# Kernel tuning notes

Hardware: AMD Instinct MI355X
Metric: run time of the kernel (lower is better)

The kernel has to match this reference:

```python
import jax, jax.numpy as jnp
import numpy as np

# Bahdanau additive attention (eval mode: dropout is identity):
#   fac1 = W @ k        [B, d, S]
#   fac2 = U @ q        [B, d, S]
#   s    = v^T tanh(fac1 + fac2)   [B, 1, S]
#   attn = softmax(s, axis=-1)

B, D, S = 32, 1024, 2048


def setup_inputs() -> dict:
    key = jax.random.key(0)
    kq, kk, kv, kW, kU = jax.random.split(key, 5)
    scale = 1.0 / np.sqrt(D)
    return {
        "q": jax.random.normal(kq, (B, D, S), dtype=jnp.float32),
        "k": jax.random.normal(kk, (B, D, S), dtype=jnp.float32),
        "v": jax.random.normal(kv, (B, D, 1), dtype=jnp.float32),
        "W": jax.random.normal(kW, (D, D), dtype=jnp.float32) * scale,
        "U": jax.random.normal(kU, (D, D), dtype=jnp.float32) * scale,
    }


def reference(q, k, v, W, U):
    # projections: [d,e] x [b,e,s] -> [b,d,s]
    fac1 = jnp.einsum("de,bes->bds", W, k)
    fac2 = jnp.einsum("de,bes->bds", U, q)
    e = jnp.tanh(fac1 + fac2)            # [B, D, S]
    s = jnp.einsum("bdo,bds->bos", v, e)  # [B, 1, S]
    attn = jax.nn.softmax(s, axis=-1)     # softmax over sequence
    return attn
```

## Files before the change

### kernel.cpp

```cpp
#include <hip/hip_runtime.h>

#define D_ 1024
#define S_ 2048
#define B_ 32
#define BM 256
#define BN 256
#define BK 64
#define NKT 32

typedef __attribute__((ext_vector_type(8))) _Float16 f16x8;
typedef __attribute__((ext_vector_type(16))) float f32x16;

__device__ __forceinline__ void async_ld16(const void* g, void* l) {
  __builtin_amdgcn_global_load_lds(
      (const __attribute__((address_space(1))) void*)g,
      (__attribute__((address_space(3))) void*)l, 16, 0, 0);
}

__global__ void prep_kernel(const float* __restrict__ W, const float* __restrict__ U,
                            _Float16* __restrict__ wf, _Float16* __restrict__ uf) {
  int t = blockIdx.x * blockDim.x + threadIdx.x;
  const float* src = blockIdx.y ? U : W;
  _Float16* dst = blockIdx.y ? uf : wf;

  int tile = t >> 11;
  int g    = t & 2047;
  int top  = g >> 6;
  int ks = top >> 3, wr = (top >> 2) & 1, fm = top & 3;
  int lane = g & 63, l31 = lane & 31, lhi = lane >> 5;
  int row   = wr * 128 + fm * 32 + l31;
  int chunk = ks * 2 + lhi;
  int d = (tile >> 4) * 256 + row;
  int e = (tile & 15) * 64 + chunk * 8;

  const float* p = src + (size_t)d * D_ + e;
  f16x8 hv;
#pragma unroll
  for (int j = 0; j < 8; ++j) hv[j] = (_Float16)p[j];
  *(f16x8*)(dst + (size_t)t * 8) = hv;
}

__global__ void __launch_bounds__(512, 2)
gemm_kernel(const float* __restrict__ kten, const float* __restrict__ qten,
            const float* __restrict__ v,
            const _Float16* __restrict__ wf, const _Float16* __restrict__ uf,
            float* __restrict__ partials) {
  __shared__ __align__(16) _Float16 Af[2][BM * BK];
  __shared__ __align__(16) _Float16 Bf[2][BN * BK];
  __shared__ float vbuf[BM];
  __shared__ float red[2][BN];

  const int tid  = threadIdx.x;
  const int lane = tid & 63;
  const int wid  = tid >> 6;
  const int wr   = wid >> 2;
  const int wc   = wid & 3;

  int bid  = blockIdx.x;
  int g    = ((bid >> 5) << 3) | (bid & 7);
  int dblk = (bid >> 3) & 3;
  int st   = g & 7;
  int b    = g >> 3;
  int s0   = st * BN;

  if (tid < BM) vbuf[tid] = v[(size_t)b * D_ + dblk * BM + tid];

  f32x16 acc[4][2];
#pragma unroll
  for (int i = 0; i < 4; ++i)
#pragma unroll
    for (int j = 0; j < 2; ++j)
#pragma unroll
      for (int r = 0; r < 16; ++r) acc[i][j][r] = 0.0f;

  const int nB = tid & 255;
  const int kq = tid >> 8;

#define PH_FENCE asm volatile("" ::: "memory")
#define PH_BAR __builtin_amdgcn_s_barrier()

#define GLLA(ktn, buf, part) do {                                              \
    const int half_ = (ktn) >> 4, ktt_ = (ktn) & 15;                           \
    const _Float16* at_ = (half_ ? uf : wf) + (size_t)(dblk * 16 + ktt_) * 16384; \
    async_ld16(at_ + (size_t)(tid + (part) * 1024) * 8,                        \
               &Af[buf][(size_t)(tid + (part) * 1024) * 8]);                   \
    async_ld16(at_ + (size_t)(tid + (part) * 1024 + 512) * 8,                  \
               &Af[buf][(size_t)(tid + (part) * 1024 + 512) * 8]);             \
  } while (0)

#define LOADB(ktn, xv, h) do {                                                 \
    const int half_ = (ktn) >> 4, ktt_ = (ktn) & 15;                           \
    const float* col_ = (half_ ? qten : kten) + (size_t)b * (D_ * S_)          \
                        + (size_t)(ktt_ * 64) * S_ + s0 + nB                   \
                        + (size_t)(kq * 32) * S_;                              \
    _Pragma("unroll")                                                          \
    for (int j = 16 * (h); j < 16 * (h) + 16; ++j) xv[j] = col_[(size_t)j * S_]; \
  } while (0)

#define CVTWRITE(xv, buf) do {                                                 \
    _Pragma("unroll")                                                          \
    for (int cl = 0; cl < 4; ++cl) {                                           \
      f16x8 hv_;                                                               \
      _Pragma("unroll")                                                        \
      for (int w = 0; w < 8; ++w) hv_[w] = (_Float16)xv[cl * 8 + w];           \
      int c_ = kq * 4 + cl, cks_ = c_ >> 1, clh_ = c_ & 1;                     \
      int gnl_ = ((cks_ * 8 + (nB >> 6) * 2 + ((nB >> 5) & 1)) << 6)           \
                 | (clh_ << 5) | (nB & 31);                                    \
      *(f16x8*)&Bf[buf][(size_t)gnl_ * 8] = hv_;                               \
    }                                                                          \
  } while (0)

#define COMPUTE_PHASE(cur_, ks_) do {                                          \
    f16x8 af_[4], bf_[2];                                                      \
    _Pragma("unroll")                                                          \
    for (int fm = 0; fm < 4; ++fm)                                             \
      af_[fm] = *(const f16x8*)&Af[cur_][(size_t)(((ks_) * 8 + wr * 4 + fm) * 64 + lane) * 8]; \
    _Pragma("unroll")                                                          \
    for (int fn = 0; fn < 2; ++fn)                                             \
      bf_[fn] = *(const f16x8*)&Bf[cur_][(size_t)(((ks_) * 8 + wc * 2 + fn) * 64 + lane) * 8]; \
    __builtin_amdgcn_s_setprio(1);                                             \
    _Pragma("unroll")                                                          \
    for (int fm = 0; fm < 4; ++fm)                                             \
      _Pragma("unroll")                                                        \
      for (int fn = 0; fn < 2; ++fn)                                           \
        acc[fm][fn] = __builtin_amdgcn_mfma_f32_32x32x16_f16(af_[fm], bf_[fn], acc[fm][fn], 0, 0, 0); \
    __builtin_amdgcn_s_setprio(0);                                             \
  } while (0)

#define STEP(kt_, cur_, xvC_, xvN_) do {                                       \
    const int nxt_ = (cur_) ^ 1;                                               \
    PH_FENCE; GLLA((kt_) + 1, nxt_, 0); COMPUTE_PHASE(cur_, 0); PH_BAR;        \
    PH_FENCE; GLLA((kt_) + 1, nxt_, 1); COMPUTE_PHASE(cur_, 1); PH_BAR;        \
    PH_FENCE; LOADB((kt_) + 2, xvN_, 0); COMPUTE_PHASE(cur_, 2); PH_BAR;       \
    PH_FENCE; LOADB((kt_) + 2, xvN_, 1); CVTWRITE(xvC_, nxt_);                 \
              COMPUTE_PHASE(cur_, 3);                                          \
    asm volatile("s_waitcnt vmcnt(32) lgkmcnt(0)" ::: "memory");               \
    PH_BAR;                                                                    \
    __builtin_amdgcn_sched_barrier(0);                                         \
  } while (0)

  float xvA[32], xvB[32];
  LOADB(0, xvA, 0); LOADB(0, xvA, 1);
  GLLA(0, 0, 0);    GLLA(0, 0, 1);
  LOADB(1, xvB, 0); LOADB(1, xvB, 1);
  CVTWRITE(xvA, 0);
  __syncthreads();

  for (int it = 0; it < 15; ++it) {
    STEP(2 * it,     0, xvB, xvA);
    STEP(2 * it + 1, 1, xvA, xvB);
  }

  PH_FENCE; GLLA(31, 1, 0); COMPUTE_PHASE(0, 0); PH_BAR;
  PH_FENCE; GLLA(31, 1, 1); COMPUTE_PHASE(0, 1); PH_BAR;
  PH_FENCE; COMPUTE_PHASE(0, 2); PH_BAR;
  PH_FENCE; CVTWRITE(xvB, 1); COMPUTE_PHASE(0, 3);
  __syncthreads();
  COMPUTE_PHASE(1, 0); COMPUTE_PHASE(1, 1); COMPUTE_PHASE(1, 2); COMPUTE_PHASE(1, 3);

#undef STEP
#undef COMPUTE_PHASE
#undef CVTWRITE
#undef LOADB
#undef GLLA
#undef PH_BAR
#undef PH_FENCE

  float psum[2] = {0.f, 0.f};
#pragma unroll
  for (int fm = 0; fm < 4; ++fm)
#pragma unroll
    for (int fn = 0; fn < 2; ++fn)
#pragma unroll
      for (int r = 0; r < 16; ++r) {
        int row = wr * 128 + fm * 32 + (r & 3) + 8 * (r >> 2) + 4 * (lane >> 5);
        float x  = acc[fm][fn][r];
        float th = 1.0f - 2.0f / (__expf(2.0f * x) + 1.0f);
        psum[fn] += vbuf[row] * th;
      }
#pragma unroll
  for (int fn = 0; fn < 2; ++fn) psum[fn] += __shfl_xor(psum[fn], 32);
  if (lane < 32) {
    red[wr][wc * 64 + lane]      = psum[0];
    red[wr][wc * 64 + 32 + lane] = psum[1];
  }
  __syncthreads();
  if (tid < BN) {
    float val = red[0][tid] + red[1][tid];
    partials[(size_t)(dblk * B_ + b) * S_ + s0 + tid] = val;
  }
}

__global__ void softmax_kernel(const float* __restrict__ partials, float* __restrict__ out) {
  __shared__ float logit[S_];
  __shared__ float wred[2][4];
  int b = blockIdx.x, tid = threadIdx.x;
  int lane = tid & 63, wid = tid >> 6;
  float lmax = -1e30f;
  for (int i = tid; i < S_; i += 256) {
    float acc = 0.f;
#pragma unroll
    for (int d = 0; d < 4; ++d) acc += partials[(size_t)(d * B_ + b) * S_ + i];
    logit[i] = acc;
    lmax = fmaxf(lmax, acc);
  }
#pragma unroll
  for (int o = 32; o; o >>= 1) lmax = fmaxf(lmax, __shfl_xor(lmax, o));
  if (lane == 0) wred[0][wid] = lmax;
  __syncthreads();
  float m = fmaxf(fmaxf(wred[0][0], wred[0][1]), fmaxf(wred[0][2], wred[0][3]));
  float lsum = 0.f;
  for (int i = tid; i < S_; i += 256) {
    float ex = __expf(logit[i] - m);
    logit[i] = ex;
    lsum += ex;
  }
#pragma unroll
  for (int o = 32; o; o >>= 1) lsum += __shfl_xor(lsum, o);
  if (lane == 0) wred[1][wid] = lsum;
  __syncthreads();
  float tot = wred[1][0] + wred[1][1] + wred[1][2] + wred[1][3];
  float inv = 1.0f / tot;
  for (int i = tid; i < S_; i += 256) out[(size_t)b * S_ + i] = logit[i] * inv;
}

extern "C" void kernel_launch(void* const* d_in, const int* in_sizes, int n_in,
                              void* d_out, int out_size, void* d_ws, size_t ws_size,
                              hipStream_t stream) {
  const float* q = (const float*)d_in[0];
  const float* k = (const float*)d_in[1];
  const float* v = (const float*)d_in[2];
  const float* W = (const float*)d_in[3];
  const float* U = (const float*)d_in[4];

  _Float16* wf = (_Float16*)d_ws;
  _Float16* uf = wf + (size_t)D_ * D_;
  float* partials = (float*)(uf + (size_t)D_ * D_);

  prep_kernel<<<dim3(512, 2), 256, 0, stream>>>(W, U, wf, uf);
  gemm_kernel<<<dim3(1024), 512, 0, stream>>>(k, q, v, wf, uf, partials);
  softmax_kernel<<<dim3(B_), 256, 0, stream>>>(partials, (float*)d_out);
}
```

Before: 401.3 us.

## Pre-convert k/q to fp16 MFMA layout and stream B tiles via async LDS loads

Adds a separate pass that converts the k and q activations to fp16 and writes them in the MFMA fragment layout in workspace. The GEMM then loads both A and B tiles with global-to-LDS async loads and a simpler double-buffered pipeline, dropping the per-thread fp32 register loads and in-kernel conversion. The cost is an extra full read of 512 MB of fp32 plus a 256 MB fp16 write and read back. The old path is kept as a fallback when the workspace is too small.

```diff
diff --git a/kernel.cpp b/kernel.cpp
--- a/kernel.cpp
+++ b/kernel.cpp
@@ -40,10 +40,32 @@
   *(f16x8*)(dst + (size_t)t * 8) = hv;
 }
 
+__global__ void kqprep_kernel(const float* __restrict__ kten, const float* __restrict__ qten,
+                              _Float16* __restrict__ bfmt) {
+  size_t t = (size_t)blockIdx.x * 256 + threadIdx.x;
+  int g    = (int)(t & 2047);
+  int tile = (int)(t >> 11);
+  int st   = tile & 7;
+  int ktt  = (tile >> 3) & 15;
+  int half = (tile >> 7) & 1;
+  int b    = tile >> 8;
+  int l31 = g & 31, clh = (g >> 5) & 1, w2 = (g >> 6) & 7, cks = g >> 9;
+  int n = w2 * 32 + l31;
+  int c = cks * 2 + clh;
+  int e = ktt * 64 + c * 8;
+  int s = st * 256 + n;
+
+  const float* src = (half ? qten : kten) + (size_t)b * (D_ * S_) + (size_t)e * S_ + s;
+  f16x8 hv;
+#pragma unroll
+  for (int j = 0; j < 8; ++j) hv[j] = (_Float16)src[(size_t)j * S_];
+  *(f16x8*)(bfmt + t * 8) = hv;
+}
+
 __global__ void __launch_bounds__(512, 2)
-gemm_kernel(const float* __restrict__ kten, const float* __restrict__ qten,
-            const float* __restrict__ v,
+gemm_kernel(const float* __restrict__ v,
             const _Float16* __restrict__ wf, const _Float16* __restrict__ uf,
+            const _Float16* __restrict__ bfmt,
             float* __restrict__ partials) {
   __shared__ __align__(16) _Float16 Af[2][BM * BK];
   __shared__ __align__(16) _Float16 Bf[2][BN * BK];
@@ -73,13 +95,9 @@
 #pragma unroll
       for (int r = 0; r < 16; ++r) acc[i][j][r] = 0.0f;
 
-  const int nB = tid & 255;
-  const int kq = tid >> 8;
-
 #define PH_FENCE asm volatile("" ::: "memory")
-#define PH_BAR __builtin_amdgcn_s_barrier()
-
-#define GLLA(ktn, buf, part) do {                                              \
+
+#define GLLA2(ktn, buf, part) do {                                             \
     const int half_ = (ktn) >> 4, ktt_ = (ktn) & 15;                           \
     const _Float16* at_ = (half_ ? uf : wf) + (size_t)(dblk * 16 + ktt_) * 16384; \
     async_ld16(at_ + (size_t)(tid + (part) * 1024) * 8,                        \
@@ -88,7 +106,142 @@
                &Af[buf][(size_t)(tid + (part) * 1024 + 512) * 8]);             \
   } while (0)
 
-#define LOADB(ktn, xv, h) do {                                                 \
+#define GLLB2(ktn, buf, part) do {                                             \
+    const int half_ = (ktn) >> 4, ktt_ = (ktn) & 15;                           \
+    const _Float16* bt_ = bfmt + ((size_t)(((b * 2 + half_) * 16 + ktt_) * 8 + st)) * 16384; \
+    async_ld16(bt_ + (size_t)(tid + (part) * 1024) * 8,                        \
+               &Bf[buf][(size_t)(tid + (part) * 1024) * 8]);                   \
+    async_ld16(bt_ + (size_t)(tid + (part) * 1024 + 512) * 8,                  \
+               &Bf[buf][(size_t)(tid + (part) * 1024 + 512) * 8]);             \
+  } while (0)
+
+#define COMPUTE_PHASE(cur_, ks_) do {                                          \
+    f16x8 af_[4], bf_[2];                                                      \
+    _Pragma("unroll")                                                          \
+    for (int fm = 0; fm < 4; ++fm)                                             \
+      af_[fm] = *(const f16x8*)&Af[cur_][(size_t)(((ks_) * 8 + wr * 4 + fm) * 64 + lane) * 8]; \
+    _Pragma("unroll")                                                          \
+    for (int fn = 0; fn < 2; ++fn)                                             \
+      bf_[fn] = *(const f16x8*)&Bf[cur_][(size_t)(((ks_) * 8 + wc * 2 + fn) * 64 + lane) * 8]; \
+    __builtin_amdgcn_s_setprio(1);                                             \
+    _Pragma("unroll")                                                          \
+    for (int fm = 0; fm < 4; ++fm)                                             \
+      _Pragma("unroll")                                                        \
+      for (int fn = 0; fn < 2; ++fn)                                           \
+        acc[fm][fn] = __builtin_amdgcn_mfma_f32_32x32x16_f16(af_[fm], bf_[fn], acc[fm][fn], 0, 0, 0); \
+    __builtin_amdgcn_s_setprio(0);                                             \
+  } while (0)
+
+#define WAIT_BAR(n) do {                                                       \
+    asm volatile("s_waitcnt vmcnt(" #n ")" ::: "memory");                      \
+    __builtin_amdgcn_s_barrier();                                              \
+    __builtin_amdgcn_sched_barrier(0);                                         \
+  } while (0)
+
+  PH_FENCE;
+  GLLA2(0, 0, 0); GLLB2(0, 0, 0);
+  GLLA2(0, 0, 1); GLLB2(0, 0, 1);
+  WAIT_BAR(4);
+
+  for (int kt = 0; kt < NKT - 1; ++kt) {
+    const int cur = kt & 1, nxt = cur ^ 1;
+    PH_FENCE;
+    GLLA2(kt + 1, nxt, 0); GLLB2(kt + 1, nxt, 0);
+    COMPUTE_PHASE(cur, 0);
+    COMPUTE_PHASE(cur, 1);
+    WAIT_BAR(4);
+    PH_FENCE;
+    GLLA2(kt + 1, nxt, 1); GLLB2(kt + 1, nxt, 1);
+    COMPUTE_PHASE(cur, 2);
+    COMPUTE_PHASE(cur, 3);
+    WAIT_BAR(4);
+  }
+  COMPUTE_PHASE(1, 0);
+  COMPUTE_PHASE(1, 1);
+  WAIT_BAR(0);
+  COMPUTE_PHASE(1, 2);
+  COMPUTE_PHASE(1, 3);
+
+#undef WAIT_BAR
+#undef COMPUTE_PHASE
+#undef GLLB2
+#undef GLLA2
+#undef PH_FENCE
+
+  float psum[2] = {0.f, 0.f};
+#pragma unroll
+  for (int fm = 0; fm < 4; ++fm)
+#pragma unroll
+    for (int fn = 0; fn < 2; ++fn)
+#pragma unroll
+      for (int r = 0; r < 16; ++r) {
+        int row = wr * 128 + fm * 32 + (r & 3) + 8 * (r >> 2) + 4 * (lane >> 5);
+        float x  = acc[fm][fn][r];
+        float th = 1.0f - 2.0f / (__expf(2.0f * x) + 1.0f);
+        psum[fn] += vbuf[row] * th;
+      }
+#pragma unroll
+  for (int fn = 0; fn < 2; ++fn) psum[fn] += __shfl_xor(psum[fn], 32);
+  if (lane < 32) {
+    red[wr][wc * 64 + lane]      = psum[0];
+    red[wr][wc * 64 + 32 + lane] = psum[1];
+  }
+  __syncthreads();
+  if (tid < BN) {
+    float val = red[0][tid] + red[1][tid];
+    partials[(size_t)(dblk * B_ + b) * S_ + s0 + tid] = val;
+  }
+}
+
+__global__ void __launch_bounds__(512, 2)
+gemm_fb_kernel(const float* __restrict__ kten, const float* __restrict__ qten,
+               const float* __restrict__ v,
+               const _Float16* __restrict__ wf, const _Float16* __restrict__ uf,
+               float* __restrict__ partials) {
+  __shared__ __align__(16) _Float16 Af[2][BM * BK];
+  __shared__ __align__(16) _Float16 Bf[2][BN * BK];
+  __shared__ float vbuf[BM];
+  __shared__ float red[2][BN];
+
+  const int tid  = threadIdx.x;
+  const int lane = tid & 63;
+  const int wid  = tid >> 6;
+  const int wr   = wid >> 2;
+  const int wc   = wid & 3;
+
+  int bid  = blockIdx.x;
+  int g    = ((bid >> 5) << 3) | (bid & 7);
+  int dblk = (bid >> 3) & 3;
+  int st   = g & 7;
+  int b    = g >> 3;
+  int s0   = st * BN;
+
+  if (tid < BM) vbuf[tid] = v[(size_t)b * D_ + dblk * BM + tid];
+
+  f32x16 acc[4][2];
+#pragma unroll
+  for (int i = 0; i < 4; ++i)
+#pragma unroll
+    for (int j = 0; j < 2; ++j)
+#pragma unroll
+      for (int r = 0; r < 16; ++r) acc[i][j][r] = 0.0f;
+
+  const int nB = tid & 255;
+  const int kq = tid >> 8;
+
+#define PH_FENCE_F asm volatile("" ::: "memory")
+#define PH_BAR_F __builtin_amdgcn_s_barrier()
+
+#define GLLA_F(ktn, buf, part) do {                                            \
+    const int half_ = (ktn) >> 4, ktt_ = (ktn) & 15;                           \
+    const _Float16* at_ = (half_ ? uf : wf) + (size_t)(dblk * 16 + ktt_) * 16384; \
+    async_ld16(at_ + (size_t)(tid + (part) * 1024) * 8,                        \
+               &Af[buf][(size_t)(tid + (part) * 1024) * 8]);                   \
+    async_ld16(at_ + (size_t)(tid + (part) * 1024 + 512) * 8,                  \
+               &Af[buf][(size_t)(tid + (part) * 1024 + 512) * 8]);             \
+  } while (0)
+
+#define LOADB_F(ktn, xv, h) do {                                               \
     const int half_ = (ktn) >> 4, ktt_ = (ktn) & 15;                           \
     const float* col_ = (half_ ? qten : kten) + (size_t)b * (D_ * S_)          \
                         + (size_t)(ktt_ * 64) * S_ + s0 + nB                   \
@@ -97,7 +250,7 @@
     for (int j = 16 * (h); j < 16 * (h) + 16; ++j) xv[j] = col_[(size_t)j * S_]; \
   } while (0)
 
-#define CVTWRITE(xv, buf) do {                                                 \
+#define CVTWRITE_F(xv, buf) do {                                               \
     _Pragma("unroll")                                                          \
     for (int cl = 0; cl < 4; ++cl) {                                           \
       f16x8 hv_;                                                               \
@@ -110,7 +263,7 @@
     }                                                                          \
   } while (0)
 
-#define COMPUTE_PHASE(cur_, ks_) do {                                          \
+#define COMPUTE_PHASE_F(cur_, ks_) do {                                        \
     f16x8 af_[4], bf_[2];                                                      \
     _Pragma("unroll")                                                          \
     for (int fm = 0; fm < 4; ++fm)                                             \
@@ -127,44 +280,44 @@
     __builtin_amdgcn_s_setprio(0);                                             \
   } while (0)
 
-#define STEP(kt_, cur_, xvC_, xvN_) do {                                       \
+#define STEP_F(kt_, cur_, xvC_, xvN_) do {                                     \
     const int nxt_ = (cur_) ^ 1;                                               \
-    PH_FENCE; GLLA((kt_) + 1, nxt_, 0); COMPUTE_PHASE(cur_, 0); PH_BAR;        \
-    PH_FENCE; GLLA((kt_) + 1, nxt_, 1); COMPUTE_PHASE(cur_, 1); PH_BAR;        \
-    PH_FENCE; LOADB((kt_) + 2, xvN_, 0); COMPUTE_PHASE(cur_, 2); PH_BAR;       \
-    PH_FENCE; LOADB((kt_) + 2, xvN_, 1); CVTWRITE(xvC_, nxt_);                 \
-              COMPUTE_PHASE(cur_, 3);                                          \
+    PH_FENCE_F; GLLA_F((kt_) + 1, nxt_, 0); COMPUTE_PHASE_F(cur_, 0); PH_BAR_F;\
+    PH_FENCE_F; GLLA_F((kt_) + 1, nxt_, 1); COMPUTE_PHASE_F(cur_, 1); PH_BAR_F;\
+    PH_FENCE_F; LOADB_F((kt_) + 2, xvN_, 0); COMPUTE_PHASE_F(cur_, 2); PH_BAR_F;\
+    PH_FENCE_F; LOADB_F((kt_) + 2, xvN_, 1); CVTWRITE_F(xvC_, nxt_);           \
+              COMPUTE_PHASE_F(cur_, 3);                                        \
     asm volatile("s_waitcnt vmcnt(32) lgkmcnt(0)" ::: "memory");               \
-    PH_BAR;                                                                    \
+    PH_BAR_F;                                                                  \
     __builtin_amdgcn_sched_barrier(0);                                         \
   } while (0)
 
   float xvA[32], xvB[32];
-  LOADB(0, xvA, 0); LOADB(0, xvA, 1);
-  GLLA(0, 0, 0);    GLLA(0, 0, 1);
-  LOADB(1, xvB, 0); LOADB(1, xvB, 1);
-  CVTWRITE(xvA, 0);
+  LOADB_F(0, xvA, 0); LOADB_F(0, xvA, 1);
+  GLLA_F(0, 0, 0);    GLLA_F(0, 0, 1);
+  LOADB_F(1, xvB, 0); LOADB_F(1, xvB, 1);
+  CVTWRITE_F(xvA, 0);
   __syncthreads();
 
   for (int it = 0; it < 15; ++it) {
-    STEP(2 * it,     0, xvB, xvA);
-    STEP(2 * it + 1, 1, xvA, xvB);
-  }
-
-  PH_FENCE; GLLA(31, 1, 0); COMPUTE_PHASE(0, 0); PH_BAR;
-  PH_FENCE; GLLA(31, 1, 1); COMPUTE_PHASE(0, 1); PH_BAR;
-  PH_FENCE; COMPUTE_PHASE(0, 2); PH_BAR;
-  PH_FENCE; CVTWRITE(xvB, 1); COMPUTE_PHASE(0, 3);
-  __syncthreads();
-  COMPUTE_PHASE(1, 0); COMPUTE_PHASE(1, 1); COMPUTE_PHASE(1, 2); COMPUTE_PHASE(1, 3);
-
-#undef STEP
-#undef COMPUTE_PHASE
-#undef CVTWRITE
-#undef LOADB
-#undef GLLA
-#undef PH_BAR
-#undef PH_FENCE
+    STEP_F(2 * it,     0, xvB, xvA);
+    STEP_F(2 * it + 1, 1, xvA, xvB);
+  }
+
+  PH_FENCE_F; GLLA_F(31, 1, 0); COMPUTE_PHASE_F(0, 0); PH_BAR_F;
+  PH_FENCE_F; GLLA_F(31, 1, 1); COMPUTE_PHASE_F(0, 1); PH_BAR_F;
+  PH_FENCE_F; COMPUTE_PHASE_F(0, 2); PH_BAR_F;
+  PH_FENCE_F; CVTWRITE_F(xvB, 1); COMPUTE_PHASE_F(0, 3);
+  __syncthreads();
+  COMPUTE_PHASE_F(1, 0); COMPUTE_PHASE_F(1, 1); COMPUTE_PHASE_F(1, 2); COMPUTE_PHASE_F(1, 3);
+
+#undef STEP_F
+#undef COMPUTE_PHASE_F
+#undef CVTWRITE_F
+#undef LOADB_F
+#undef GLLA_F
+#undef PH_BAR_F
+#undef PH_FENCE_F
 
   float psum[2] = {0.f, 0.f};
 #pragma unroll
@@ -236,8 +389,15 @@
   _Float16* wf = (_Float16*)d_ws;
   _Float16* uf = wf + (size_t)D_ * D_;
   float* partials = (float*)(uf + (size_t)D_ * D_);
+  _Float16* bfmt = (_Float16*)((char*)d_ws + 5242880);
+  const size_t NEED = 5242880ull + 268435456ull;
 
   prep_kernel<<<dim3(512, 2), 256, 0, stream>>>(W, U, wf, uf);
-  gemm_kernel<<<dim3(1024), 512, 0, stream>>>(k, q, v, wf, uf, partials);
+  if (ws_size >= NEED) {
+    kqprep_kernel<<<dim3(65536), 256, 0, stream>>>(k, q, bfmt);
+    gemm_kernel<<<dim3(1024), 512, 0, stream>>>(v, wf, uf, bfmt, partials);
+  } else {
+    gemm_fb_kernel<<<dim3(1024), 512, 0, stream>>>(k, q, v, wf, uf, partials);
+  }
   softmax_kernel<<<dim3(B_), 256, 0, stream>>>(partials, (float*)d_out);
 }
```

Measured after the change: 441.9 us. +10.1%, slower.
